# Kernel optimization log

Measured on AMD Instinct MI355X. Metric: run time of the kernel, lower is better.

The kernel has to match this reference:

```python
import jax, jax.numpy as jnp
import numpy as np

N = 100000   # nodes
F_IN = 128   # node features
H = 32       # hidden size (hard-coded in module)


def setup_inputs() -> dict:
    key = jax.random.key(0)
    ks = jax.random.split(key, 20)
    inp = {
        'x': jax.random.normal(ks[0], (N, F_IN), dtype=jnp.float32),
        'edge_index': jax.random.randint(ks[1], (2, 3200000), 0, N, dtype=jnp.int64),
        'edge_weight': jax.random.uniform(ks[2], (3200000,), dtype=jnp.float32),
        'prev_hidden_state': jax.random.normal(ks[3], (N, H), dtype=jnp.float32),
    }
    s = 1.0 / np.sqrt(F_IN)
    s2 = 1.0 / np.sqrt(2 * H)
    sh = 1.0 / np.sqrt(H)
    # GCNConv weights (in->H) + bias, for gates z, r, h
    for i, g in enumerate(['z', 'r', 'h']):
        inp[f'Wc_{g}'] = jax.random.uniform(ks[4 + i], (F_IN, H), minval=-s, maxval=s, dtype=jnp.float32)
        inp[f'bc_{g}'] = jnp.zeros((H,), dtype=jnp.float32)
        # torch Linear(2H -> H): weight [H, 2H], bias [H]
        inp[f'Wl_{g}'] = jax.random.uniform(ks[8 + i], (H, 2 * H), minval=-s2, maxval=s2, dtype=jnp.float32)
        inp[f'bl_{g}'] = jax.random.uniform(ks[12 + i], (H,), minval=-s2, maxval=s2, dtype=jnp.float32)
    inp['W_head'] = jax.random.uniform(ks[16], (1, H), minval=-sh, maxval=sh, dtype=jnp.float32)
    inp['b_head'] = jax.random.uniform(ks[17], (1,), minval=-sh, maxval=sh, dtype=jnp.float32)
    return inp


def _gcn_norm(edge_index, edge_weight):
    # add self-loops with weight 1, symmetric GCN normalization
    loop = jnp.arange(N, dtype=edge_index.dtype)
    row = jnp.concatenate([edge_index[0], loop])
    col = jnp.concatenate([edge_index[1], loop])
    w = jnp.concatenate([edge_weight, jnp.ones((N,), dtype=edge_weight.dtype)])
    deg = jax.ops.segment_sum(w, col, num_segments=N)
    dinv = jnp.where(deg > 0, jax.lax.rsqrt(jnp.where(deg > 0, deg, 1.0)), 0.0)
    norm = dinv[row] * w * dinv[col]
    return row, col, norm


def _gcn_conv(x, W, b, row, col, norm):
    xw = x @ W                                   # [N, H]
    agg = jax.ops.segment_sum(norm[:, None] * xw[row], col, num_segments=N)
    return agg + b


def reference(x, edge_index, edge_weight, prev_hidden_state,
              Wc_z, bc_z, Wl_z, bl_z,
              Wc_r, bc_r, Wl_r, bl_r,
              Wc_h, bc_h, Wl_h, bl_h,
              W_head, b_head):
    row, col, norm = _gcn_norm(edge_index, edge_weight)
    Hprev = prev_hidden_state

    cz = _gcn_conv(x, Wc_z, bc_z, row, col, norm)
    Z = jax.nn.sigmoid(jnp.concatenate([cz, Hprev], axis=1) @ Wl_z.T + bl_z)

    cr = _gcn_conv(x, Wc_r, bc_r, row, col, norm)
    R = jax.nn.sigmoid(jnp.concatenate([cr, Hprev], axis=1) @ Wl_r.T + bl_r)

    ch = _gcn_conv(x, Wc_h, bc_h, row, col, norm)
    Ht = jnp.tanh(jnp.concatenate([ch, Hprev * R], axis=1) @ Wl_h.T + bl_h)

    Hnew = Z * Hprev + (1.0 - Z) * Ht
    y = jax.nn.relu(Hnew) @ W_head.T + b_head    # [N, 1]
    return (y, Hnew)
```

## Files before the change

### kernel.cpp

```cpp
#include <hip/hip_runtime.h>

#define NN 100000
#define FIN 128
#define HD 32
#define EE 3200000
#define NBUK 391
#define EPB 6144
#define NBLK ((EE + EPB - 1) / EPB)

typedef unsigned int uint;
typedef unsigned short ushort;

__device__ __forceinline__ ushort f2bf(float f) {
    uint b = __float_as_uint(f);
    return (ushort)((b + 0x7FFFu + ((b >> 16) & 1u)) >> 16);
}
__device__ __forceinline__ float bf2f(ushort u) {
    return __uint_as_float(((uint)u) << 16);
}

__global__ void detect_kernel(const uint* __restrict__ ei32, int* __restrict__ flag) {
    int t = threadIdx.x;
    uint v = 0;
#pragma unroll
    for (int r = 0; r < 4; r++) v |= ei32[2 * (t + 64 * r) + 1];
    unsigned long long nz = __ballot(v != 0u);
    if (t == 0) *flag = (nz == 0ULL) ? 1 : 0;
}

__device__ __forceinline__ int load_idx32(const int* __restrict__ ei, long long pos, int is64) {
    return is64 ? ei[pos * 2] : ei[pos];
}

__global__ __launch_bounds__(256) void passA_hist(const int* __restrict__ ei,
                                                  int* __restrict__ blockhist,
                                                  const int* __restrict__ flag) {
    __shared__ int hist[NBUK];
    int tid = threadIdx.x, blk = blockIdx.x;
    for (int b = tid; b < NBUK; b += 256) hist[b] = 0;
    __syncthreads();
    int is64 = *flag;
    int e0 = blk * EPB, e1 = e0 + EPB; if (e1 > EE) e1 = EE;
    for (int e = e0 + tid; e < e1; e += 256) {
        int col = load_idx32(ei, (long long)EE + e, is64);
        atomicAdd(&hist[col >> 8], 1);
    }
    __syncthreads();
    for (int b = tid; b < NBUK; b += 256) blockhist[blk * NBUK + b] = hist[b];
}

__global__ void scan_bucket(const int* __restrict__ blockhist, int* __restrict__ off_local,
                            int* __restrict__ total) {
    int b = blockIdx.x;
    int l = threadIdx.x;
    int run = 0;
    for (int c = 0; c < NBLK; c += 64) {
        int blk = c + l;
        int v = (blk < NBLK) ? blockhist[blk * NBUK + b] : 0;
        int incl = v;
#pragma unroll
        for (int d = 1; d < 64; d <<= 1) {
            int t = __shfl_up(incl, d, 64);
            if (l >= d) incl += t;
        }
        if (blk < NBLK) off_local[blk * NBUK + b] = run + (incl - v);
        run += __shfl(incl, 63, 64);
    }
    if (l == 0) total[b] = run;
}

__global__ void scan_total(const int* __restrict__ total, int* __restrict__ bstart) {
    __shared__ int sd[512];
    int t = threadIdx.x;
    int v = (t < NBUK) ? total[t] : 0;
    sd[t] = v;
    __syncthreads();
    for (int off = 1; off < 512; off <<= 1) {
        int x = (t >= off) ? sd[t - off] : 0;
        __syncthreads();
        sd[t] += x;
        __syncthreads();
    }
    if (t < NBUK) bstart[t] = sd[t] - v;
    if (t == NBUK - 1) bstart[NBUK] = sd[t];
}

__global__ __launch_bounds__(256) void sortC_kernel(const int* __restrict__ ei,
                                                    const float* __restrict__ wt,
                                                    const int* __restrict__ bstart,
                                                    const int* __restrict__ off_local,
                                                    const int* __restrict__ blockhist,
                                                    uint2* __restrict__ erec2,
                                                    const int* __restrict__ flag) {
    __shared__ uint2 lrec[EPB];
    __shared__ int lstart[NBUK];
    __shared__ int lcur[NBUK];
    int tid = threadIdx.x, blk = blockIdx.x;
    if (tid < 64) {
        int run = 0;
        for (int c = 0; c < NBUK; c += 64) {
            int b = c + tid;
            int v = (b < NBUK) ? blockhist[blk * NBUK + b] : 0;
            int incl = v;
#pragma unroll
            for (int d = 1; d < 64; d <<= 1) {
                int t2 = __shfl_up(incl, d, 64);
                if (tid >= d) incl += t2;
            }
            if (b < NBUK) { lstart[b] = run + incl - v; lcur[b] = run + incl - v; }
            run += __shfl(incl, 63, 64);
        }
    }
    __syncthreads();
    int is64 = *flag;
    int e0 = blk * EPB, e1 = e0 + EPB; if (e1 > EE) e1 = EE;
    for (int e = e0 + tid; e < e1; e += 256) {
        int row = load_idx32(ei, e, is64);
        int col = load_idx32(ei, (long long)EE + e, is64);
        uint nb = __float_as_uint(wt[e]);
        uint enc = ((nb + 0x8000u) >> 16) & 0x7FFFu;
        int pos = atomicAdd(&lcur[col >> 8], 1);
        uint2 r; r.x = (uint)row | (enc << 17); r.y = (uint)col;
        lrec[pos] = r;
    }
    __syncthreads();
    int m = e1 - e0;
    for (int slot = tid; slot < m; slot += 256) {
        uint2 r = lrec[slot];
        int b = (int)(r.y >> 8);
        int gpos = bstart[b] + off_local[blk * NBUK + b] + (slot - lstart[b]);
        erec2[gpos] = r;
    }
}

__global__ __launch_bounds__(256) void passB_fine(const uint2* __restrict__ erec2,
                                                  const int* __restrict__ bstart,
                                                  uint* __restrict__ erecF,
                                                  int* __restrict__ estart, int* __restrict__ cnt,
                                                  float* __restrict__ dinv) {
    __shared__ int hist[256];
    __shared__ float wsum[256];
    __shared__ int off[256];
    __shared__ int cur[256];
    __shared__ int sd[256];
    int t = threadIdx.x, b = blockIdx.x;
    hist[t] = 0; wsum[t] = 0.f;
    __syncthreads();
    int e0 = bstart[b], e1 = bstart[b + 1];
    for (int e = e0 + t; e < e1; e += 256) {
        uint2 r = erec2[e];
        int cl = (int)(r.y & 255u);
        atomicAdd(&hist[cl], 1);
        atomicAdd(&wsum[cl], __uint_as_float((r.x >> 17) << 16));
    }
    __syncthreads();
    int v = hist[t];
    sd[t] = v;
    __syncthreads();
    for (int o = 1; o < 256; o <<= 1) {
        int x = (t >= o) ? sd[t - o] : 0;
        __syncthreads();
        sd[t] += x;
        __syncthreads();
    }
    off[t] = sd[t] - v;
    cur[t] = 0;
    int node = b * 256 + t;
    if (node < NN) {
        estart[node] = e0 + off[t];
        cnt[node] = v;
        dinv[node] = rsqrtf(1.0f + wsum[t]);
    }
    __syncthreads();
    for (int e = e0 + t; e < e1; e += 256) {
        uint2 r = erec2[e];
        int cl = (int)(r.y & 255u);
        int p = atomicAdd(&cur[cl], 1);
        erecF[e0 + off[cl] + p] = r.x;
    }
}

__global__ void fixup_kernel(uint* __restrict__ erecF, const float* __restrict__ dinv) {
    int e = blockIdx.x * blockDim.x + threadIdx.x;
    if (e >= EE) return;
    uint v = erecF[e];
    int row = (int)(v & 0x1FFFFu);
    float w = __uint_as_float((v >> 17) << 16);
    float wd = w * dinv[row];
    uint nb = __float_as_uint(wd);
    uint enc = ((nb + 0x8000u) >> 16) & 0x7FFFu;
    erecF[e] = (uint)row | (enc << 17);
}

__global__ __launch_bounds__(256) void gemm_xw_kernel(
        const float* __restrict__ x,
        const float* __restrict__ Wz, const float* __restrict__ Wr, const float* __restrict__ Wh,
        ushort* __restrict__ xw16) {
    __shared__ float Bs[128 * 96];
    __shared__ float AsT[8 * 128];
    int tid = threadIdx.x;
    int tx = tid & 31, ty = tid >> 5;
    int rowBase = blockIdx.x * 128;

    for (int e = tid; e < 4096; e += 256) { int k = e >> 5, c = e & 31; Bs[k * 96 + c]      = Wz[e]; }
    for (int e = tid; e < 4096; e += 256) { int k = e >> 5, c = e & 31; Bs[k * 96 + 32 + c] = Wr[e]; }
    for (int e = tid; e < 4096; e += 256) { int k = e >> 5, c = e & 31; Bs[k * 96 + 64 + c] = Wh[e]; }

    float acc0[16], acc1[16], acc2[16];
#pragma unroll
    for (int r = 0; r < 16; r++) { acc0[r] = 0.f; acc1[r] = 0.f; acc2[r] = 0.f; }

    int lr = tid >> 1;
    int lc = (tid & 1) * 4;
    for (int k0 = 0; k0 < 128; k0 += 8) {
        __syncthreads();
        int gr = rowBase + lr;
        float4 a4 = make_float4(0.f, 0.f, 0.f, 0.f);
        if (gr < NN) a4 = *(const float4*)(x + (long long)gr * FIN + k0 + lc);
        AsT[(lc + 0) * 128 + lr] = a4.x;
        AsT[(lc + 1) * 128 + lr] = a4.y;
        AsT[(lc + 2) * 128 + lr] = a4.z;
        AsT[(lc + 3) * 128 + lr] = a4.w;
        __syncthreads();
#pragma unroll
        for (int kk = 0; kk < 8; kk++) {
            float b0 = Bs[(k0 + kk) * 96 + tx];
            float b1 = Bs[(k0 + kk) * 96 + 32 + tx];
            float b2 = Bs[(k0 + kk) * 96 + 64 + tx];
            const float4* ap = (const float4*)(AsT + kk * 128 + ty * 16);
            float4 a0 = ap[0], a1 = ap[1], a2 = ap[2], a3 = ap[3];
            float av[16] = {a0.x,a0.y,a0.z,a0.w, a1.x,a1.y,a1.z,a1.w,
                            a2.x,a2.y,a2.z,a2.w, a3.x,a3.y,a3.z,a3.w};
#pragma unroll
            for (int r = 0; r < 16; r++) {
                acc0[r] = fmaf(av[r], b0, acc0[r]);
                acc1[r] = fmaf(av[r], b1, acc1[r]);
                acc2[r] = fmaf(av[r], b2, acc2[r]);
            }
        }
    }
#pragma unroll
    for (int r = 0; r < 16; r++) {
        int gr = rowBase + ty * 16 + r;
        if (gr < NN) {
            ushort* o = xw16 + (long long)gr * 96;
            uint zr = (uint)f2bf(acc0[r]) | ((uint)f2bf(acc1[r]) << 16);
            *(uint*)(o + 2 * tx) = zr;
            o[64 + tx] = f2bf(acc2[r]);
        }
    }
}

__global__ __launch_bounds__(512) void agg_gate_kernel(
        const uint* __restrict__ erecF, const int* __restrict__ estart, const int* __restrict__ cnt,
        const ushort* __restrict__ xw16, const float* __restrict__ dinv,
        const float* __restrict__ hprev,
        const float* __restrict__ bcz, const float* __restrict__ bcr, const float* __restrict__ bch,
        const float* __restrict__ Wlz, const float* __restrict__ blz,
        const float* __restrict__ Wlr, const float* __restrict__ blr,
        const float* __restrict__ Wlh, const float* __restrict__ blh,
        const float* __restrict__ Whead, const float* __restrict__ bhead,
        float* __restrict__ y, float* __restrict__ hnew) {
    __shared__ float WzT[64 * 32], WrT[64 * 32], WhT[64 * 32];
    __shared__ float czs[16][32], crs[16][32], chs[16][32], hps[16][32], rhs[16][32];
    __shared__ uint rwsh[16][32];
    int tid = threadIdx.x;
    for (int e2 = tid; e2 < 2048; e2 += 512) {
        int jj = e2 >> 6, k = e2 & 63;
        WzT[k * 32 + jj] = Wlz[e2];
        WrT[k * 32 + jj] = Wlr[e2];
        WhT[k * 32 + jj] = Wlh[e2];
    }
    int s = tid >> 5, j = tid & 31;
    int i = blockIdx.x * 16 + s;
    int beg = estart[i], c = cnt[i], end = beg + c;

    float cz = 0.f, cr = 0.f, ch = 0.f;
    int e = beg + j;
    uint vcur = (e < end) ? erecF[e] : 0u;
    for (int base = beg; base < end; base += 32) {
        rwsh[s][j] = vcur;
        int en = base + 32 + j;
        uint vnext = (en < end) ? erecF[en] : 0u;
        int mm = end - base; if (mm > 32) mm = 32;
        int t = 0;
        for (; t + 4 <= mm; t += 4) {
            uint v0 = rwsh[s][t], v1 = rwsh[s][t + 1], v2 = rwsh[s][t + 2], v3 = rwsh[s][t + 3];
            const ushort* p0 = xw16 + (long long)(v0 & 0x1FFFFu) * 96;
            const ushort* p1 = xw16 + (long long)(v1 & 0x1FFFFu) * 96;
            const ushort* p2 = xw16 + (long long)(v2 & 0x1FFFFu) * 96;
            const ushort* p3 = xw16 + (long long)(v3 & 0x1FFFFu) * 96;
            uint a0 = *(const uint*)(p0 + 2 * j);
            uint a1 = *(const uint*)(p1 + 2 * j);
            uint a2 = *(const uint*)(p2 + 2 * j);
            uint a3 = *(const uint*)(p3 + 2 * j);
            ushort h0 = p0[64 + j], h1 = p1[64 + j], h2 = p2[64 + j], h3 = p3[64 + j];
            float w0 = __uint_as_float((v0 >> 17) << 16);
            float w1 = __uint_as_float((v1 >> 17) << 16);
            float w2 = __uint_as_float((v2 >> 17) << 16);
            float w3 = __uint_as_float((v3 >> 17) << 16);
            cz = fmaf(w0, __uint_as_float(a0 << 16), cz);
            cr = fmaf(w0, __uint_as_float(a0 & 0xFFFF0000u), cr);
            ch = fmaf(w0, bf2f(h0), ch);
            cz = fmaf(w1, __uint_as_float(a1 << 16), cz);
            cr = fmaf(w1, __uint_as_float(a1 & 0xFFFF0000u), cr);
            ch = fmaf(w1, bf2f(h1), ch);
            cz = fmaf(w2, __uint_as_float(a2 << 16), cz);
            cr = fmaf(w2, __uint_as_float(a2 & 0xFFFF0000u), cr);
            ch = fmaf(w2, bf2f(h2), ch);
            cz = fmaf(w3, __uint_as_float(a3 << 16), cz);
            cr = fmaf(w3, __uint_as_float(a3 & 0xFFFF0000u), cr);
            ch = fmaf(w3, bf2f(h3), ch);
        }
        for (; t < mm; t++) {
            uint v = rwsh[s][t];
            const ushort* xr = xw16 + (long long)(v & 0x1FFFFu) * 96;
            uint zr = *(const uint*)(xr + 2 * j);
            float fh = bf2f(xr[64 + j]);
            float w = __uint_as_float((v >> 17) << 16);
            cz = fmaf(w, __uint_as_float(zr << 16), cz);
            cr = fmaf(w, __uint_as_float(zr & 0xFFFF0000u), cr);
            ch = fmaf(w, fh, ch);
        }
        vcur = vnext;
    }
    float di = dinv[i], sl = di * di;
    const ushort* xi = xw16 + (long long)i * 96;
    uint zri = *(const uint*)(xi + 2 * j);
    czs[s][j] = fmaf(sl, __uint_as_float(zri << 16),         di * cz) + bcz[j];
    crs[s][j] = fmaf(sl, __uint_as_float(zri & 0xFFFF0000u), di * cr) + bcr[j];
    chs[s][j] = fmaf(sl, bf2f(xi[64 + j]),                   di * ch) + bch[j];
    float hp = hprev[(long long)i * HD + j];
    hps[s][j] = hp;
    __syncthreads();

    float az = blz[j], arv = blr[j];
#pragma unroll
    for (int k = 0; k < 32; k++) {
        az  = fmaf(WzT[k * 32 + j], czs[s][k], az);
        arv = fmaf(WrT[k * 32 + j], crs[s][k], arv);
    }
#pragma unroll
    for (int k = 0; k < 32; k++) {
        float v = hps[s][k];
        az  = fmaf(WzT[(k + 32) * 32 + j], v, az);
        arv = fmaf(WrT[(k + 32) * 32 + j], v, arv);
    }
    float Z = 1.f / (1.f + __expf(-az));
    float R = 1.f / (1.f + __expf(-arv));
    rhs[s][j] = hp * R;
    __syncthreads();

    float ah = blh[j];
#pragma unroll
    for (int k = 0; k < 32; k++) ah = fmaf(WhT[k * 32 + j], chs[s][k], ah);
#pragma unroll
    for (int k = 0; k < 32; k++) ah = fmaf(WhT[(k + 32) * 32 + j], rhs[s][k], ah);
    float Ht = tanhf(ah);
    float hn = Z * hp + (1.f - Z) * Ht;
    float yv = fmaxf(hn, 0.f) * Whead[j];
#pragma unroll
    for (int m = 16; m; m >>= 1) yv += __shfl_xor(yv, m, 32);
    hnew[(long long)i * HD + j] = hn;
    if (j == 0) y[i] = yv + bhead[0];
}

extern "C" void kernel_launch(void* const* d_in, const int* in_sizes, int n_in,
                              void* d_out, int out_size, void* d_ws, size_t ws_size,
                              hipStream_t stream) {
    const float* x     = (const float*)d_in[0];
    const int*   ei    = (const int*)d_in[1];
    const float* wt    = (const float*)d_in[2];
    const float* hprev = (const float*)d_in[3];
    const float* Wcz = (const float*)d_in[4],  *bcz = (const float*)d_in[5];
    const float* Wlz = (const float*)d_in[6],  *blz = (const float*)d_in[7];
    const float* Wcr = (const float*)d_in[8],  *bcr = (const float*)d_in[9];
    const float* Wlr = (const float*)d_in[10], *blr = (const float*)d_in[11];
    const float* Wch = (const float*)d_in[12], *bch = (const float*)d_in[13];
    const float* Wlh = (const float*)d_in[14], *blh = (const float*)d_in[15];
    const float* Whead = (const float*)d_in[16], *bhead = (const float*)d_in[17];

    float* out_y = (float*)d_out;
    float* out_h = (float*)d_out + NN;

    float* ws = (float*)d_ws;
    float* dinv      = ws;
    int*   estart    = (int*)(ws + NN);
    int*   cnt       = (int*)(ws + 2LL * NN);
    int*   bstart    = (int*)(ws + 3LL * NN);
    int*   total     = (int*)(ws + 3LL * NN + 512);
    int*   blockhist = (int*)(ws + 3LL * NN + 1024);
    int*   off_local = (int*)(ws + 3LL * NN + 205024);
    int*   flag      = (int*)(ws + 3LL * NN + 409024);
    ushort* xw16     = (ushort*)(ws + 3LL * NN + 409056);
    uint2*  erec2    = (uint2*)(ws + 51LL * NN + 409056);
    uint*   erecF    = (uint*)(ws + 51LL * NN + 409056 + 2LL * EE);

    detect_kernel<<<1, 64, 0, stream>>>((const uint*)ei, flag);
    passA_hist<<<NBLK, 256, 0, stream>>>(ei, blockhist, flag);
    scan_bucket<<<NBUK, 64, 0, stream>>>(blockhist, off_local, total);
    scan_total<<<1, 512, 0, stream>>>(total, bstart);
    sortC_kernel<<<NBLK, 256, 0, stream>>>(ei, wt, bstart, off_local, blockhist, erec2, flag);
    passB_fine<<<NBUK, 256, 0, stream>>>(erec2, bstart, erecF, estart, cnt, dinv);
    gemm_xw_kernel<<<(NN + 127) / 128, 256, 0, stream>>>(x, Wcz, Wcr, Wch, xw16);
    fixup_kernel<<<(EE + 255) / 256, 256, 0, stream>>>(erecF, dinv);
    agg_gate_kernel<<<NN / 16, 512, 0, stream>>>(
        erecF, estart, cnt, xw16, dinv, hprev, bcz, bcr, bch,
        Wlz, blz, Wlr, blr, Wlh, blh, Whead, bhead, out_y, out_h);
}
```

Measured before the change: 459.3 us.

## Fold dinv scaling into the xw GEMM, drop the fixup and detect kernels, and widen sort kernels

The per-source dinv factor moves out of the edge records: the xw GEMM epilogue now scales each row by dinv before bf16 packing. That removes the fixup kernel, which read and rewrote every edge record. The int64-detection kernel is merged into passA_hist. sortC and passB_fine run with 512 threads, and sortC precomputes a combined scatter offset per bucket. The aggregation loop is unrolled by 8 with byte-offset addressing, several loads and stores become nontemporal, and two __syncthreads are removed from the gate stage, which relies on each node's 32 lanes sharing one wavefront.

Result: slower. 689.7 us (+50.2%).

```diff
diff --git a/kernel.cpp b/kernel.cpp
--- a/kernel.cpp
+++ b/kernel.cpp
@@ -10,6 +10,7 @@
 
 typedef unsigned int uint;
 typedef unsigned short ushort;
+typedef float vfloat4 __attribute__((ext_vector_type(4)));
 
 __device__ __forceinline__ ushort f2bf(float f) {
     uint b = __float_as_uint(f);
@@ -19,27 +20,28 @@
     return __uint_as_float(((uint)u) << 16);
 }
 
-__global__ void detect_kernel(const uint* __restrict__ ei32, int* __restrict__ flag) {
-    int t = threadIdx.x;
-    uint v = 0;
-#pragma unroll
-    for (int r = 0; r < 4; r++) v |= ei32[2 * (t + 64 * r) + 1];
-    unsigned long long nz = __ballot(v != 0u);
-    if (t == 0) *flag = (nz == 0ULL) ? 1 : 0;
-}
-
 __device__ __forceinline__ int load_idx32(const int* __restrict__ ei, long long pos, int is64) {
-    return is64 ? ei[pos * 2] : ei[pos];
+    return is64 ? __builtin_nontemporal_load(ei + pos * 2)
+                : __builtin_nontemporal_load(ei + pos);
 }
 
 __global__ __launch_bounds__(256) void passA_hist(const int* __restrict__ ei,
                                                   int* __restrict__ blockhist,
-                                                  const int* __restrict__ flag) {
+                                                  int* __restrict__ flag) {
     __shared__ int hist[NBUK];
+    __shared__ int sis64;
     int tid = threadIdx.x, blk = blockIdx.x;
     for (int b = tid; b < NBUK; b += 256) hist[b] = 0;
-    __syncthreads();
-    int is64 = *flag;
+    if (tid < 64) {
+        uint v = 0;
+#pragma unroll
+        for (int r = 0; r < 4; r++) v |= ((const uint*)ei)[2 * (tid + 64 * r) + 1];
+        unsigned long long nz = __ballot(v != 0u);
+        if (tid == 0) sis64 = (nz == 0ULL) ? 1 : 0;
+    }
+    __syncthreads();
+    int is64 = sis64;
+    if (blk == 0 && tid == 0) *flag = is64;
     int e0 = blk * EPB, e1 = e0 + EPB; if (e1 > EE) e1 = EE;
     for (int e = e0 + tid; e < e1; e += 256) {
         int col = load_idx32(ei, (long long)EE + e, is64);
@@ -85,7 +87,7 @@
     if (t == NBUK - 1) bstart[NBUK] = sd[t];
 }
 
-__global__ __launch_bounds__(256) void sortC_kernel(const int* __restrict__ ei,
+__global__ __launch_bounds__(512) void sortC_kernel(const int* __restrict__ ei,
                                                     const float* __restrict__ wt,
                                                     const int* __restrict__ bstart,
                                                     const int* __restrict__ off_local,
@@ -93,7 +95,7 @@
                                                     uint2* __restrict__ erec2,
                                                     const int* __restrict__ flag) {
     __shared__ uint2 lrec[EPB];
-    __shared__ int lstart[NBUK];
+    __shared__ int lcombo[NBUK];
     __shared__ int lcur[NBUK];
     int tid = threadIdx.x, blk = blockIdx.x;
     if (tid < 64) {
@@ -107,17 +109,21 @@
                 int t2 = __shfl_up(incl, d, 64);
                 if (tid >= d) incl += t2;
             }
-            if (b < NBUK) { lstart[b] = run + incl - v; lcur[b] = run + incl - v; }
+            if (b < NBUK) {
+                int ls = run + incl - v;
+                lcur[b] = ls;
+                lcombo[b] = bstart[b] + off_local[blk * NBUK + b] - ls;
+            }
             run += __shfl(incl, 63, 64);
         }
     }
     __syncthreads();
     int is64 = *flag;
     int e0 = blk * EPB, e1 = e0 + EPB; if (e1 > EE) e1 = EE;
-    for (int e = e0 + tid; e < e1; e += 256) {
+    for (int e = e0 + tid; e < e1; e += 512) {
         int row = load_idx32(ei, e, is64);
         int col = load_idx32(ei, (long long)EE + e, is64);
-        uint nb = __float_as_uint(wt[e]);
+        uint nb = __float_as_uint(__builtin_nontemporal_load(wt + e));
         uint enc = ((nb + 0x8000u) >> 16) & 0x7FFFu;
         int pos = atomicAdd(&lcur[col >> 8], 1);
         uint2 r; r.x = (uint)row | (enc << 17); r.y = (uint)col;
@@ -125,15 +131,14 @@
     }
     __syncthreads();
     int m = e1 - e0;
-    for (int slot = tid; slot < m; slot += 256) {
+    for (int slot = tid; slot < m; slot += 512) {
         uint2 r = lrec[slot];
-        int b = (int)(r.y >> 8);
-        int gpos = bstart[b] + off_local[blk * NBUK + b] + (slot - lstart[b]);
+        int gpos = lcombo[r.y >> 8] + slot;
         erec2[gpos] = r;
     }
 }
 
-__global__ __launch_bounds__(256) void passB_fine(const uint2* __restrict__ erec2,
+__global__ __launch_bounds__(512) void passB_fine(const uint2* __restrict__ erec2,
                                                   const int* __restrict__ bstart,
                                                   uint* __restrict__ erecF,
                                                   int* __restrict__ estart, int* __restrict__ cnt,
@@ -144,35 +149,37 @@
     __shared__ int cur[256];
     __shared__ int sd[256];
     int t = threadIdx.x, b = blockIdx.x;
-    hist[t] = 0; wsum[t] = 0.f;
+    if (t < 256) { hist[t] = 0; wsum[t] = 0.f; }
     __syncthreads();
     int e0 = bstart[b], e1 = bstart[b + 1];
-    for (int e = e0 + t; e < e1; e += 256) {
+    for (int e = e0 + t; e < e1; e += 512) {
         uint2 r = erec2[e];
         int cl = (int)(r.y & 255u);
         atomicAdd(&hist[cl], 1);
         atomicAdd(&wsum[cl], __uint_as_float((r.x >> 17) << 16));
     }
     __syncthreads();
-    int v = hist[t];
-    sd[t] = v;
+    int v = 0;
+    if (t < 256) { v = hist[t]; sd[t] = v; }
     __syncthreads();
     for (int o = 1; o < 256; o <<= 1) {
-        int x = (t >= o) ? sd[t - o] : 0;
-        __syncthreads();
-        sd[t] += x;
-        __syncthreads();
-    }
-    off[t] = sd[t] - v;
-    cur[t] = 0;
-    int node = b * 256 + t;
-    if (node < NN) {
-        estart[node] = e0 + off[t];
-        cnt[node] = v;
-        dinv[node] = rsqrtf(1.0f + wsum[t]);
-    }
-    __syncthreads();
-    for (int e = e0 + t; e < e1; e += 256) {
+        int x = (t >= o && t < 256) ? sd[t - o] : 0;
+        __syncthreads();
+        if (t < 256) sd[t] += x;
+        __syncthreads();
+    }
+    if (t < 256) {
+        off[t] = sd[t] - v;
+        cur[t] = 0;
+        int node = b * 256 + t;
+        if (node < NN) {
+            estart[node] = e0 + off[t];
+            cnt[node] = v;
+            dinv[node] = rsqrtf(1.0f + wsum[t]);
+        }
+    }
+    __syncthreads();
+    for (int e = e0 + t; e < e1; e += 512) {
         uint2 r = erec2[e];
         int cl = (int)(r.y & 255u);
         int p = atomicAdd(&cur[cl], 1);
@@ -180,21 +187,10 @@
     }
 }
 
-__global__ void fixup_kernel(uint* __restrict__ erecF, const float* __restrict__ dinv) {
-    int e = blockIdx.x * blockDim.x + threadIdx.x;
-    if (e >= EE) return;
-    uint v = erecF[e];
-    int row = (int)(v & 0x1FFFFu);
-    float w = __uint_as_float((v >> 17) << 16);
-    float wd = w * dinv[row];
-    uint nb = __float_as_uint(wd);
-    uint enc = ((nb + 0x8000u) >> 16) & 0x7FFFu;
-    erecF[e] = (uint)row | (enc << 17);
-}
-
 __global__ __launch_bounds__(256) void gemm_xw_kernel(
         const float* __restrict__ x,
         const float* __restrict__ Wz, const float* __restrict__ Wr, const float* __restrict__ Wh,
+        const float* __restrict__ dinv,
         ushort* __restrict__ xw16) {
     __shared__ float Bs[128 * 96];
     __shared__ float AsT[8 * 128];
@@ -215,8 +211,8 @@
     for (int k0 = 0; k0 < 128; k0 += 8) {
         __syncthreads();
         int gr = rowBase + lr;
-        float4 a4 = make_float4(0.f, 0.f, 0.f, 0.f);
-        if (gr < NN) a4 = *(const float4*)(x + (long long)gr * FIN + k0 + lc);
+        vfloat4 a4 = (vfloat4)(0.f);
+        if (gr < NN) a4 = __builtin_nontemporal_load((const vfloat4*)(x + (long long)gr * FIN + k0 + lc));
         AsT[(lc + 0) * 128 + lr] = a4.x;
         AsT[(lc + 1) * 128 + lr] = a4.y;
         AsT[(lc + 2) * 128 + lr] = a4.z;
@@ -243,15 +239,16 @@
     for (int r = 0; r < 16; r++) {
         int gr = rowBase + ty * 16 + r;
         if (gr < NN) {
+            float di = dinv[gr];
             ushort* o = xw16 + (long long)gr * 96;
-            uint zr = (uint)f2bf(acc0[r]) | ((uint)f2bf(acc1[r]) << 16);
+            uint zr = (uint)f2bf(acc0[r] * di) | ((uint)f2bf(acc1[r] * di) << 16);
             *(uint*)(o + 2 * tx) = zr;
-            o[64 + tx] = f2bf(acc2[r]);
-        }
-    }
-}
-
-__global__ __launch_bounds__(512) void agg_gate_kernel(
+            o[64 + tx] = f2bf(acc2[r] * di);
+        }
+    }
+}
+
+__global__ __launch_bounds__(512, 8) void agg_gate_kernel(
         const uint* __restrict__ erecF, const int* __restrict__ estart, const int* __restrict__ cnt,
         const ushort* __restrict__ xw16, const float* __restrict__ dinv,
         const float* __restrict__ hprev,
@@ -275,64 +272,89 @@
     int i = blockIdx.x * 16 + s;
     int beg = estart[i], c = cnt[i], end = beg + c;
 
+    const char* xwb = (const char*)xw16;
+    uint jo4 = 4u * (uint)j;
+    uint jo2 = 128u + 2u * (uint)j;
+
     float cz = 0.f, cr = 0.f, ch = 0.f;
     int e = beg + j;
-    uint vcur = (e < end) ? erecF[e] : 0u;
+    uint vcur = (e < end) ? __builtin_nontemporal_load(erecF + e) : 0u;
+    __syncthreads();
+
+#define REC(vv, aa, hh)                                                    \
+    {                                                                      \
+        float w_ = __uint_as_float(((vv) >> 17) << 16);                    \
+        cz = fmaf(w_, __uint_as_float((aa) << 16), cz);                    \
+        cr = fmaf(w_, __uint_as_float((aa) & 0xFFFF0000u), cr);            \
+        ch = fmaf(w_, bf2f(hh), ch);                                       \
+    }
+
     for (int base = beg; base < end; base += 32) {
         rwsh[s][j] = vcur;
         int en = base + 32 + j;
-        uint vnext = (en < end) ? erecF[en] : 0u;
+        uint vnext = (en < end) ? __builtin_nontemporal_load(erecF + en) : 0u;
         int mm = end - base; if (mm > 32) mm = 32;
         int t = 0;
+        for (; t + 8 <= mm; t += 8) {
+            uint v0 = rwsh[s][t + 0], v1 = rwsh[s][t + 1], v2 = rwsh[s][t + 2], v3 = rwsh[s][t + 3];
+            uint v4 = rwsh[s][t + 4], v5 = rwsh[s][t + 5], v6 = rwsh[s][t + 6], v7 = rwsh[s][t + 7];
+            uint b0 = (v0 & 0x1FFFFu) * 192u, b1 = (v1 & 0x1FFFFu) * 192u;
+            uint b2 = (v2 & 0x1FFFFu) * 192u, b3 = (v3 & 0x1FFFFu) * 192u;
+            uint b4 = (v4 & 0x1FFFFu) * 192u, b5 = (v5 & 0x1FFFFu) * 192u;
+            uint b6 = (v6 & 0x1FFFFu) * 192u, b7 = (v7 & 0x1FFFFu) * 192u;
+            uint a0 = *(const uint*)(xwb + b0 + jo4);
+            uint a1 = *(const uint*)(xwb + b1 + jo4);
+            uint a2 = *(const uint*)(xwb + b2 + jo4);
+            uint a3 = *(const uint*)(xwb + b3 + jo4);
+            uint a4 = *(const uint*)(xwb + b4 + jo4);
+            uint a5 = *(const uint*)(xwb + b5 + jo4);
+            uint a6 = *(const uint*)(xwb + b6 + jo4);
+            uint a7 = *(const uint*)(xwb + b7 + jo4);
+            ushort h0 = *(const ushort*)(xwb + b0 + jo2);
+            ushort h1 = *(const ushort*)(xwb + b1 + jo2);
+            ushort h2 = *(const ushort*)(xwb + b2 + jo2);
+            ushort h3 = *(const ushort*)(xwb + b3 + jo2);
+            ushort h4 = *(const ushort*)(xwb + b4 + jo2);
+            ushort h5 = *(const ushort*)(xwb + b5 + jo2);
+            ushort h6 = *(const ushort*)(xwb + b6 + jo2);
+            ushort h7 = *(const ushort*)(xwb + b7 + jo2);
+            REC(v0, a0, h0) REC(v1, a1, h1) REC(v2, a2, h2) REC(v3, a3, h3)
+            REC(v4, a4, h4) REC(v5, a5, h5) REC(v6, a6, h6) REC(v7, a7, h7)
+        }
         for (; t + 4 <= mm; t += 4) {
-            uint v0 = rwsh[s][t], v1 = rwsh[s][t + 1], v2 = rwsh[s][t + 2], v3 = rwsh[s][t + 3];
-            const ushort* p0 = xw16 + (long long)(v0 & 0x1FFFFu) * 96;
-            const ushort* p1 = xw16 + (long long)(v1 & 0x1FFFFu) * 96;
-            const ushort* p2 = xw16 + (long long)(v2 & 0x1FFFFu) * 96;
-            const ushort* p3 = xw16 + (long long)(v3 & 0x1FFFFu) * 96;
-            uint a0 = *(const uint*)(p0 + 2 * j);
-            uint a1 = *(const uint*)(p1 + 2 * j);
-            uint a2 = *(const uint*)(p2 + 2 * j);
-            uint a3 = *(const uint*)(p3 + 2 * j);
-            ushort h0 = p0[64 + j], h1 = p1[64 + j], h2 = p2[64 + j], h3 = p3[64 + j];
-            float w0 = __uint_as_float((v0 >> 17) << 16);
-            float w1 = __uint_as_float((v1 >> 17) << 16);
-            float w2 = __uint_as_float((v2 >> 17) << 16);
-            float w3 = __uint_as_float((v3 >> 17) << 16);
-            cz = fmaf(w0, __uint_as_float(a0 << 16), cz);
-            cr = fmaf(w0, __uint_as_float(a0 & 0xFFFF0000u), cr);
-            ch = fmaf(w0, bf2f(h0), ch);
-            cz = fmaf(w1, __uint_as_float(a1 << 16), cz);
-            cr = fmaf(w1, __uint_as_float(a1 & 0xFFFF0000u), cr);
-            ch = fmaf(w1, bf2f(h1), ch);
-            cz = fmaf(w2, __uint_as_float(a2 << 16), cz);
-            cr = fmaf(w2, __uint_as_float(a2 & 0xFFFF0000u), cr);
-            ch = fmaf(w2, bf2f(h2), ch);
-            cz = fmaf(w3, __uint_as_float(a3 << 16), cz);
-            cr = fmaf(w3, __uint_as_float(a3 & 0xFFFF0000u), cr);
-            ch = fmaf(w3, bf2f(h3), ch);
+            uint v0 = rwsh[s][t + 0], v1 = rwsh[s][t + 1], v2 = rwsh[s][t + 2], v3 = rwsh[s][t + 3];
+            uint b0 = (v0 & 0x1FFFFu) * 192u, b1 = (v1 & 0x1FFFFu) * 192u;
+            uint b2 = (v2 & 0x1FFFFu) * 192u, b3 = (v3 & 0x1FFFFu) * 192u;
+            uint a0 = *(const uint*)(xwb + b0 + jo4);
+            uint a1 = *(const uint*)(xwb + b1 + jo4);
+            uint a2 = *(const uint*)(xwb + b2 + jo4);
+            uint a3 = *(const uint*)(xwb + b3 + jo4);
+            ushort h0 = *(const ushort*)(xwb + b0 + jo2);
+            ushort h1 = *(const ushort*)(xwb + b1 + jo2);
+            ushort h2 = *(const ushort*)(xwb + b2 + jo2);
+            ushort h3 = *(const ushort*)(xwb + b3 + jo2);
+            REC(v0, a0, h0) REC(v1, a1, h1) REC(v2, a2, h2) REC(v3, a3, h3)
         }
         for (; t < mm; t++) {
-            uint v = rwsh[s][t];
-            const ushort* xr = xw16 + (long long)(v & 0x1FFFFu) * 96;
-            uint zr = *(const uint*)(xr + 2 * j);
-            float fh = bf2f(xr[64 + j]);
-            float w = __uint_as_float((v >> 17) << 16);
-            cz = fmaf(w, __uint_as_float(zr << 16), cz);
-            cr = fmaf(w, __uint_as_float(zr & 0xFFFF0000u), cr);
-            ch = fmaf(w, fh, ch);
+            uint v0 = rwsh[s][t];
+            uint b0 = (v0 & 0x1FFFFu) * 192u;
+            uint a0 = *(const uint*)(xwb + b0 + jo4);
+            ushort h0 = *(const ushort*)(xwb + b0 + jo2);
+            REC(v0, a0, h0)
         }
         vcur = vnext;
     }
-    float di = dinv[i], sl = di * di;
-    const ushort* xi = xw16 + (long long)i * 96;
-    uint zri = *(const uint*)(xi + 2 * j);
-    czs[s][j] = fmaf(sl, __uint_as_float(zri << 16),         di * cz) + bcz[j];
-    crs[s][j] = fmaf(sl, __uint_as_float(zri & 0xFFFF0000u), di * cr) + bcr[j];
-    chs[s][j] = fmaf(sl, bf2f(xi[64 + j]),                   di * ch) + bch[j];
-    float hp = hprev[(long long)i * HD + j];
+#undef REC
+
+    float di = dinv[i];
+    uint bi = (uint)i * 192u;
+    uint zri = *(const uint*)(xwb + bi + jo4);
+    float hself = bf2f(*(const ushort*)(xwb + bi + jo2));
+    czs[s][j] = fmaf(di, cz + __uint_as_float(zri << 16), bcz[j]);
+    crs[s][j] = fmaf(di, cr + __uint_as_float(zri & 0xFFFF0000u), bcr[j]);
+    chs[s][j] = fmaf(di, ch + hself, bch[j]);
+    float hp = __builtin_nontemporal_load(hprev + (long long)i * HD + j);
     hps[s][j] = hp;
-    __syncthreads();
 
     float az = blz[j], arv = blr[j];
 #pragma unroll
@@ -349,7 +371,6 @@
     float Z = 1.f / (1.f + __expf(-az));
     float R = 1.f / (1.f + __expf(-arv));
     rhs[s][j] = hp * R;
-    __syncthreads();
 
     float ah = blh[j];
 #pragma unroll
@@ -361,7 +382,7 @@
     float yv = fmaxf(hn, 0.f) * Whead[j];
 #pragma unroll
     for (int m = 16; m; m >>= 1) yv += __shfl_xor(yv, m, 32);
-    hnew[(long long)i * HD + j] = hn;
+    __builtin_nontemporal_store(hn, hnew + (long long)i * HD + j);
     if (j == 0) y[i] = yv + bhead[0];
 }
 
@@ -396,14 +417,12 @@
     uint2*  erec2    = (uint2*)(ws + 51LL * NN + 409056);
     uint*   erecF    = (uint*)(ws + 51LL * NN + 409056 + 2LL * EE);
 
-    detect_kernel<<<1, 64, 0, stream>>>((const uint*)ei, flag);
     passA_hist<<<NBLK, 256, 0, stream>>>(ei, blockhist, flag);
     scan_bucket<<<NBUK, 64, 0, stream>>>(blockhist, off_local, total);
     scan_total<<<1, 512, 0, stream>>>(total, bstart);
-    sortC_kernel<<<NBLK, 256, 0, stream>>>(ei, wt, bstart, off_local, blockhist, erec2, flag);
-    passB_fine<<<NBUK, 256, 0, stream>>>(erec2, bstart, erecF, estart, cnt, dinv);
-    gemm_xw_kernel<<<(NN + 127) / 128, 256, 0, stream>>>(x, Wcz, Wcr, Wch, xw16);
-    fixup_kernel<<<(EE + 255) / 256, 256, 0, stream>>>(erecF, dinv);
+    sortC_kernel<<<NBLK, 512, 0, stream>>>(ei, wt, bstart, off_local, blockhist, erec2, flag);
+    passB_fine<<<NBUK, 512, 0, stream>>>(erec2, bstart, erecF, estart, cnt, dinv);
+    gemm_xw_kernel<<<(NN + 127) / 128, 256, 0, stream>>>(x, Wcz, Wcr, Wch, dinv, xw16);
     agg_gate_kernel<<<NN / 16, 512, 0, stream>>>(
         erecF, estart, cnt, xw16, dinv, hprev, bcz, bcr, bch,
         Wlz, blz, Wlr, blr, Wlh, blh, Whead, bhead, out_y, out_h);
```
